# Optimization experiments

Hardware: AMD Instinct MI355X
Metric: run time of the kernel (lower is better)

The kernel has to match this reference:

```python
import jax, jax.numpy as jnp
import numpy as np

BETA = 0.25


def setup_inputs() -> dict:
    key = jax.random.key(0)
    k1, k2 = jax.random.split(key)
    ze = jax.random.normal(k1, (16, 64, 64, 64), dtype=jnp.float32)  # (B, L, H, W)
    # codebook init mirrors uniform_(-1/K, 1/K)
    K = 1024
    emb = jax.random.uniform(k2, (K, 64), dtype=jnp.float32, minval=-1.0 / K, maxval=1.0 / K)
    return {"ze": ze, "emb": emb}


def reference(ze, emb):
    B, L, H, W = ze.shape
    K = emb.shape[0]
    # (B, H, W, L) -> (N, L)
    zf = jnp.transpose(ze, (0, 2, 3, 1)).reshape(-1, L)
    # squared euclidean distances (N, K)
    d = (jnp.sum(zf * zf, axis=1, keepdims=True)
         + jnp.sum(emb * emb, axis=1)
         - 2.0 * zf @ emb.T)
    idx = jnp.argmin(d, axis=1)  # (N,)
    # direct gather == one-hot @ emb
    z_q = jnp.transpose(emb[idx].reshape(B, H, W, L), (0, 3, 1, 2))
    loss = (jnp.mean((jax.lax.stop_gradient(z_q) - ze) ** 2)
            + BETA * jnp.mean((z_q - jax.lax.stop_gradient(ze)) ** 2))
    # straight-through estimator
    z_q_st = ze + jax.lax.stop_gradient(z_q - ze)
    # perplexity of code usage
    counts = jnp.zeros((K,), dtype=zf.dtype).at[idx].add(1.0)
    e_mean = counts / zf.shape[0]
    perplexity = jnp.exp(-jnp.sum(e_mean * jnp.log(e_mean + 1e-10)))
    return z_q_st, loss, idx.reshape(-1, 1)
```

## Files before the change

kernel.cpp:

```cpp
#include <hip/hip_runtime.h>

typedef short bf16x8 __attribute__((ext_vector_type(8)));
typedef float f32x4  __attribute__((ext_vector_type(4)));

#define CAP 12

#define WS_LOSS 0
#define WS_DONE 8
#define WS_EN   64
#define WS_EBF  4160

#define L_EBF    0
#define L_MARG   131072
#define L_CCNT   132096
#define L_KCH    133120
#define L_CSLOT  134144
#define L_TOTAL  146432

__device__ __forceinline__ unsigned short f2bf(float f) {
    unsigned u = __float_as_uint(f);
    return (unsigned short)((u + 0x7fffu + ((u >> 16) & 1u)) >> 16);
}

__device__ __forceinline__ float np_pairwise_sumsq64(const float* a) {
    float r[8];
    #pragma unroll
    for (int j = 0; j < 8; ++j) r[j] = __fmul_rn(a[j], a[j]);
    #pragma unroll
    for (int i = 8; i < 64; i += 8)
        #pragma unroll
        for (int j = 0; j < 8; ++j)
            r[j] = __fadd_rn(r[j], __fmul_rn(a[i + j], a[i + j]));
    return __fadd_rn(
        __fadd_rn(__fadd_rn(r[0], r[1]), __fadd_rn(r[2], r[3])),
        __fadd_rn(__fadd_rn(r[4], r[5]), __fadd_rn(r[6], r[7])));
}

__global__ __launch_bounds__(256) void prep_kernel(
    const float* __restrict__ emb, unsigned short* __restrict__ ebf,
    float* __restrict__ en_t,
    float* __restrict__ loss, int* __restrict__ done)
{
    int k = blockIdx.x * 256 + threadIdx.x;
    if (k == 0) { *loss = 0.0f; *done = 0; }
    if (k < 1024) {
        float e[64];
        #pragma unroll
        for (int l = 0; l < 64; ++l) e[l] = emb[k * 64 + l];
        en_t[k] = np_pairwise_sumsq64(e);
        int tile = k >> 4, r = k & 15;
        #pragma unroll
        for (int j = 0; j < 8; ++j) {
            bf16x8 v;
            #pragma unroll
            for (int m = 0; m < 8; ++m) v[m] = (short)f2bf(e[j * 8 + m]);
            *(bf16x8*)(ebf + tile * 1024 + j * 128 + r * 8) = v;
        }
    }
}

__global__ __launch_bounds__(512, 2)
void vq_kernel(
    const float* __restrict__ ze, const float* __restrict__ emb,
    const unsigned short* __restrict__ ebf, const float* __restrict__ en_t,
    float* __restrict__ out_zq, float* __restrict__ out_idxf,
    float* __restrict__ loss, int* __restrict__ done,
    float* __restrict__ out_loss)
{
    extern __shared__ char smem[];
    unsigned short* ebf_l = (unsigned short*)(smem + L_EBF);
    float*          marg_l= (float*)(smem + L_MARG);
    int*            ccnt  = (int*)(smem + L_CCNT);
    int*            kch   = (int*)(smem + L_KCH);
    int*            cslot = (int*)(smem + L_CSLOT);

    const int t = threadIdx.x;
    const int n0 = blockIdx.x * 256;
    const int gbase = (n0 >> 12) * 262144 + (n0 & 4095);

    {
        const bf16x8* src = (const bf16x8*)ebf;
        bf16x8* dst = (bf16x8*)ebf_l;
        #pragma unroll 16
        for (int i = 0; i < 16; ++i) dst[t + i * 512] = src[t + i * 512];
    }

    const int wv = t >> 6, lane = t & 63;
    const int r = lane & 15, q = lane >> 4;
    const int wp = wv * 32;
    bf16x8 a[2][2];
    float sm[2] = {0.f, 0.f};
    #pragma unroll
    for (int rg = 0; rg < 2; ++rg) {
        const float* zb = ze + gbase + wp + rg * 16 + r;
        #pragma unroll
        for (int j = 0; j < 8; ++j) {
            const float v0 = zb[(q * 8 + j) * 4096];
            const float v1 = zb[(32 + q * 8 + j) * 4096];
            a[rg][0][j] = (short)f2bf(v0);
            a[rg][1][j] = (short)f2bf(v1);
            sm[rg] += fabsf(v0) + fabsf(v1);
        }
    }
    #pragma unroll
    for (int rg = 0; rg < 2; ++rg) {
        float s = sm[rg];
        s += __shfl_xor(s, 16, 64);
        s += __shfl_xor(s, 32, 64);
        if (q == 0) marg_l[wp + rg * 16 + r] = 1.67e-5f * s + 2.0e-4f;
    }
    if (t < 256) ccnt[t] = 0;
    __syncthreads();

    const unsigned short* bptr = ebf_l + q * 128 + r * 8;

    float rm[8];
    #pragma unroll
    for (int i = 0; i < 8; ++i) rm[i] = -1e30f;
    {
        bf16x8 pb0[8], pb1[8];
        #pragma unroll
        for (int i = 0; i < 8; ++i) {
            pb0[i] = *(const bf16x8*)(bptr + i * 1024);
            pb1[i] = *(const bf16x8*)(bptr + i * 1024 + 512);
        }
        #pragma unroll 8
        for (int tile = 0; tile < 64; ++tile) {
            bf16x8 b0 = pb0[tile & 7], b1 = pb1[tile & 7];
            int nt = tile + 8; if (nt > 63) nt = 63;
            pb0[tile & 7] = *(const bf16x8*)(bptr + nt * 1024);
            pb1[tile & 7] = *(const bf16x8*)(bptr + nt * 1024 + 512);
            #pragma unroll
            for (int rg = 0; rg < 2; ++rg) {
                f32x4 c = {0.f, 0.f, 0.f, 0.f};
                c = __builtin_amdgcn_mfma_f32_16x16x32_bf16(a[rg][0], b0, c, 0, 0, 0);
                c = __builtin_amdgcn_mfma_f32_16x16x32_bf16(a[rg][1], b1, c, 0, 0, 0);
                #pragma unroll
                for (int i = 0; i < 4; ++i)
                    rm[rg * 4 + i] = fmaxf(rm[rg * 4 + i], c[i]);
            }
        }
    }
    #pragma unroll
    for (int j = 0; j < 8; ++j) {
        float v = rm[j];
        v = fmaxf(v, __shfl_xor(v, 1, 16));
        v = fmaxf(v, __shfl_xor(v, 2, 16));
        v = fmaxf(v, __shfl_xor(v, 4, 16));
        v = fmaxf(v, __shfl_xor(v, 8, 16));
        rm[j] = v;
    }
    float thr[8];
    #pragma unroll
    for (int j = 0; j < 8; ++j) {
        const int row = wp + (j >> 2) * 16 + q * 4 + (j & 3);
        thr[j] = rm[j] - 0.5f * marg_l[row];
    }

    float z[64];
    {
        const int p = t >> 1;
        const float* zp = ze + gbase + p;
        #pragma unroll
        for (int l = 0; l < 64; ++l) z[l] = zp[l * 4096];
    }

    {
        bf16x8 pb0[8], pb1[8];
        #pragma unroll
        for (int i = 0; i < 8; ++i) {
            pb0[i] = *(const bf16x8*)(bptr + i * 1024);
            pb1[i] = *(const bf16x8*)(bptr + i * 1024 + 512);
        }
        #pragma unroll 8
        for (int tile = 0; tile < 64; ++tile) {
            bf16x8 b0 = pb0[tile & 7], b1 = pb1[tile & 7];
            int nt = tile + 8; if (nt > 63) nt = 63;
            pb0[tile & 7] = *(const bf16x8*)(bptr + nt * 1024);
            pb1[tile & 7] = *(const bf16x8*)(bptr + nt * 1024 + 512);
            const int code = tile * 16 + r;
            #pragma unroll
            for (int rg = 0; rg < 2; ++rg) {
                f32x4 c = {0.f, 0.f, 0.f, 0.f};
                c = __builtin_amdgcn_mfma_f32_16x16x32_bf16(a[rg][0], b0, c, 0, 0, 0);
                c = __builtin_amdgcn_mfma_f32_16x16x32_bf16(a[rg][1], b1, c, 0, 0, 0);
                #pragma unroll
                for (int i = 0; i < 4; ++i) {
                    if (c[i] >= thr[rg * 4 + i]) {
                        const int pp = wp + rg * 16 + q * 4 + i;
                        const int ci = atomicAdd(&ccnt[pp], 1);
                        if (ci < CAP) cslot[pp * CAP + ci] = code;
                    }
                }
            }
        }
    }
    __syncthreads();

    {
        const int p = t >> 1, cl = t & 1;
        int cnt = ccnt[p]; if (cnt > CAP) cnt = CAP;
        const float znorm = np_pairwise_sumsq64(z);
        float best = 1e30f; int bk = 1 << 20;
        int kcur = (cl < cnt) ? cslot[p * CAP + cl] : 0;
        for (int c = cl; c < cnt; c += 2) {
            const int k = kcur;
            const int ni = c + 2;
            kcur = (ni < cnt) ? cslot[p * CAP + ni] : 0;
            const float4* er = (const float4*)(emb + k * 64);
            float acc = 0.0f;
            #pragma unroll
            for (int jj = 0; jj < 16; ++jj) {
                const float4 v = er[jj];
                acc = fmaf(z[4 * jj + 0], v.x, acc);
                acc = fmaf(z[4 * jj + 1], v.y, acc);
                acc = fmaf(z[4 * jj + 2], v.z, acc);
                acc = fmaf(z[4 * jj + 3], v.w, acc);
            }
            const float sc = __fsub_rn(__fadd_rn(znorm, en_t[k]), __fmul_rn(2.0f, acc));
            if (sc < best || (sc == best && k < bk)) { best = sc; bk = k; }
        }
        const float ob = __shfl_xor(best, 1, 64);
        const int   ok = __shfl_xor(bk, 1, 64);
        if (ob < best || (ob == best && ok < bk)) { best = ob; bk = ok; }
        if (cl == 0) {
            kch[p] = bk;
            out_idxf[n0 + p] = (float)bk;
        }
    }
    __syncthreads();

    {
        const int p = t & 255, h = t >> 8;
        const int bk = kch[p];
        const float* er = emb + bk * 64 + h * 32;
        const float* zp = ze + gbase + p + (h * 32) * 4096;
        float* op = out_zq + gbase + p + (h * 32) * 4096;
        float ev[32], zv[32];
        #pragma unroll
        for (int j = 0; j < 32; ++j) ev[j] = er[j];
        #pragma unroll
        for (int j = 0; j < 32; ++j) zv[j] = zp[j * 4096];
        float ls = 0.0f;
        #pragma unroll
        for (int j = 0; j < 32; ++j) {
            op[j * 4096] = ev[j];
            const float d = ev[j] - zv[j];
            ls = fmaf(d, d, ls);
        }
        #pragma unroll
        for (int off = 32; off > 0; off >>= 1) ls += __shfl_down(ls, off, 64);
        if (lane == 0) atomicAdd(loss, ls);
    }

    __syncthreads();
    if (t == 0) {
        __threadfence();
        int old = atomicAdd(done, 1);
        if (old == (int)gridDim.x - 1) {
            __threadfence();
            float total = atomicAdd(loss, 0.0f);
            *out_loss = 1.25f * total / 4194304.0f;
        }
    }
}

extern "C" void kernel_launch(void* const* d_in, const int* in_sizes, int n_in,
                              void* d_out, int out_size, void* d_ws, size_t ws_size,
                              hipStream_t stream)
{
    const float* ze  = (const float*)d_in[0];
    const float* emb = (const float*)d_in[1];
    float* out = (float*)d_out;
    float* out_zq   = out;
    float* out_loss = out + 4194304;
    float* out_idxf = out + 4194305;

    char* w = (char*)d_ws;
    float*          ws_loss = (float*)(w + WS_LOSS);
    int*            ws_done = (int*)(w + WS_DONE);
    float*          ws_en   = (float*)(w + WS_EN);
    unsigned short* ebf     = (unsigned short*)(w + WS_EBF);

    static bool attr_set = false;
    if (!attr_set) {
        hipFuncSetAttribute((const void*)vq_kernel,
                            hipFuncAttributeMaxDynamicSharedMemorySize, L_TOTAL);
        attr_set = true;
    }

    prep_kernel<<<4, 256, 0, stream>>>(emb, ebf, ws_en, ws_loss, ws_done);
    vq_kernel<<<256, 512, L_TOTAL, stream>>>(ze, emb, ebf, ws_en, out_zq,
                                             out_idxf, ws_loss, ws_done, out_loss);
}
```

Before: 138.2 us.

## Split fused VQ kernel into distance, rescore, and epilogue kernels

The single fused kernel becomes three launches: a bf16 MFMA candidate-filter kernel that writes per-point candidate lists to global scratch (aliased into the z_q output buffer), an fp32 rescore kernel with one thread per point, and an epilogue that gathers codes, writes z_q and reduces the loss. This removes the 64-float z register array from the MFMA kernel and lets each phase use its own launch shape and occupancy. The cost is extra launches, a global round trip for candidate slots and indices, and a second read of ze.

```diff
diff --git a/kernel.cpp b/kernel.cpp
--- a/kernel.cpp
+++ b/kernel.cpp
@@ -10,12 +10,14 @@
 #define WS_EN   64
 #define WS_EBF  4160
 
-#define L_EBF    0
-#define L_MARG   131072
-#define L_CCNT   132096
-#define L_KCH    133120
-#define L_CSLOT  134144
-#define L_TOTAL  146432
+#define SLOT_OFF 0
+#define CNT_OFF  786432
+
+#define LD_EBF    0
+#define LD_MARG   131072
+#define LD_CCNT   132096
+#define LD_CSLOT  133120
+#define LD_TOTAL  145408
 
 __device__ __forceinline__ unsigned short f2bf(float f) {
     unsigned u = __float_as_uint(f);
@@ -60,19 +62,15 @@
 }
 
 __global__ __launch_bounds__(512, 2)
-void vq_kernel(
-    const float* __restrict__ ze, const float* __restrict__ emb,
-    const unsigned short* __restrict__ ebf, const float* __restrict__ en_t,
-    float* __restrict__ out_zq, float* __restrict__ out_idxf,
-    float* __restrict__ loss, int* __restrict__ done,
-    float* __restrict__ out_loss)
+void dist_kernel(
+    const float* __restrict__ ze, const unsigned short* __restrict__ ebf,
+    int* __restrict__ slot_g, int* __restrict__ cnt_g)
 {
     extern __shared__ char smem[];
-    unsigned short* ebf_l = (unsigned short*)(smem + L_EBF);
-    float*          marg_l= (float*)(smem + L_MARG);
-    int*            ccnt  = (int*)(smem + L_CCNT);
-    int*            kch   = (int*)(smem + L_KCH);
-    int*            cslot = (int*)(smem + L_CSLOT);
+    unsigned short* ebf_l = (unsigned short*)(smem + LD_EBF);
+    float*          marg_l= (float*)(smem + LD_MARG);
+    int*            ccnt  = (int*)(smem + LD_CCNT);
+    int*            cslot = (int*)(smem + LD_CSLOT);
 
     const int t = threadIdx.x;
     const int n0 = blockIdx.x * 256;
@@ -155,14 +153,6 @@
     for (int j = 0; j < 8; ++j) {
         const int row = wp + (j >> 2) * 16 + q * 4 + (j & 3);
         thr[j] = rm[j] - 0.5f * marg_l[row];
-    }
-
-    float z[64];
-    {
-        const int p = t >> 1;
-        const float* zp = ze + gbase + p;
-        #pragma unroll
-        for (int l = 0; l < 64; ++l) z[l] = zp[l * 4096];
     }
 
     {
@@ -197,61 +187,78 @@
     }
     __syncthreads();
 
-    {
-        const int p = t >> 1, cl = t & 1;
-        int cnt = ccnt[p]; if (cnt > CAP) cnt = CAP;
-        const float znorm = np_pairwise_sumsq64(z);
-        float best = 1e30f; int bk = 1 << 20;
-        int kcur = (cl < cnt) ? cslot[p * CAP + cl] : 0;
-        for (int c = cl; c < cnt; c += 2) {
-            const int k = kcur;
-            const int ni = c + 2;
-            kcur = (ni < cnt) ? cslot[p * CAP + ni] : 0;
-            const float4* er = (const float4*)(emb + k * 64);
-            float acc = 0.0f;
-            #pragma unroll
-            for (int jj = 0; jj < 16; ++jj) {
-                const float4 v = er[jj];
-                acc = fmaf(z[4 * jj + 0], v.x, acc);
-                acc = fmaf(z[4 * jj + 1], v.y, acc);
-                acc = fmaf(z[4 * jj + 2], v.z, acc);
-                acc = fmaf(z[4 * jj + 3], v.w, acc);
-            }
-            const float sc = __fsub_rn(__fadd_rn(znorm, en_t[k]), __fmul_rn(2.0f, acc));
-            if (sc < best || (sc == best && k < bk)) { best = sc; bk = k; }
-        }
-        const float ob = __shfl_xor(best, 1, 64);
-        const int   ok = __shfl_xor(bk, 1, 64);
-        if (ob < best || (ob == best && ok < bk)) { best = ob; bk = ok; }
-        if (cl == 0) {
-            kch[p] = bk;
-            out_idxf[n0 + p] = (float)bk;
-        }
-    }
-    __syncthreads();
-
-    {
-        const int p = t & 255, h = t >> 8;
-        const int bk = kch[p];
-        const float* er = emb + bk * 64 + h * 32;
-        const float* zp = ze + gbase + p + (h * 32) * 4096;
-        float* op = out_zq + gbase + p + (h * 32) * 4096;
-        float ev[32], zv[32];
-        #pragma unroll
-        for (int j = 0; j < 32; ++j) ev[j] = er[j];
-        #pragma unroll
-        for (int j = 0; j < 32; ++j) zv[j] = zp[j * 4096];
-        float ls = 0.0f;
-        #pragma unroll
-        for (int j = 0; j < 32; ++j) {
-            op[j * 4096] = ev[j];
-            const float d = ev[j] - zv[j];
-            ls = fmaf(d, d, ls);
-        }
-        #pragma unroll
-        for (int off = 32; off > 0; off >>= 1) ls += __shfl_down(ls, off, 64);
-        if (lane == 0) atomicAdd(loss, ls);
-    }
+    if (t < 256) {
+        const int P = n0 + t;
+        cnt_g[P] = ccnt[t];
+        const int4* s = (const int4*)(cslot + t * CAP);
+        int4* d = (int4*)(slot_g + P * CAP);
+        d[0] = s[0]; d[1] = s[1]; d[2] = s[2];
+    }
+}
+
+__global__ __launch_bounds__(256, 4)
+void rescore_kernel(
+    const float* __restrict__ ze, const float* __restrict__ emb,
+    const float* __restrict__ en_t,
+    const int* __restrict__ slot_g, const int* __restrict__ cnt_g,
+    float* __restrict__ out_idxf)
+{
+    const int P = blockIdx.x * 256 + threadIdx.x;
+    int cnt = cnt_g[P]; if (cnt > CAP) cnt = CAP;
+    const float* zp = ze + (P >> 12) * 262144 + (P & 4095);
+    float z[64];
+    #pragma unroll
+    for (int l = 0; l < 64; ++l) z[l] = zp[l * 4096];
+    const float znorm = np_pairwise_sumsq64(z);
+    float best = 1e30f; int bk = 1 << 20;
+    for (int c = 0; c < cnt; ++c) {
+        const int k = slot_g[P * CAP + c];
+        const float4* er = (const float4*)(emb + k * 64);
+        float acc = 0.0f;
+        #pragma unroll
+        for (int jj = 0; jj < 16; ++jj) {
+            const float4 v = er[jj];
+            acc = fmaf(z[4 * jj + 0], v.x, acc);
+            acc = fmaf(z[4 * jj + 1], v.y, acc);
+            acc = fmaf(z[4 * jj + 2], v.z, acc);
+            acc = fmaf(z[4 * jj + 3], v.w, acc);
+        }
+        const float sc = __fsub_rn(__fadd_rn(znorm, en_t[k]), __fmul_rn(2.0f, acc));
+        if (sc < best || (sc == best && k < bk)) { best = sc; bk = k; }
+    }
+    out_idxf[P] = (float)bk;
+}
+
+__global__ __launch_bounds__(512, 2)
+void epi_kernel(
+    const float* __restrict__ ze, const float* __restrict__ emb,
+    const float* __restrict__ out_idxf,
+    float* __restrict__ out_zq, float* __restrict__ loss,
+    int* __restrict__ done, float* __restrict__ out_loss)
+{
+    const int t = threadIdx.x, lane = t & 63;
+    const int n0 = blockIdx.x * 256;
+    const int gbase = (n0 >> 12) * 262144 + (n0 & 4095);
+    const int p = t & 255, h = t >> 8;
+    const int bk = (int)out_idxf[n0 + p];
+    const float* er = emb + bk * 64 + h * 32;
+    const float* zp = ze + gbase + p + (h * 32) * 4096;
+    float* op = out_zq + gbase + p + (h * 32) * 4096;
+    float ev[32], zv[32];
+    #pragma unroll
+    for (int j = 0; j < 32; ++j) ev[j] = er[j];
+    #pragma unroll
+    for (int j = 0; j < 32; ++j) zv[j] = zp[j * 4096];
+    float ls = 0.0f;
+    #pragma unroll
+    for (int j = 0; j < 32; ++j) {
+        op[j * 4096] = ev[j];
+        const float d = ev[j] - zv[j];
+        ls = fmaf(d, d, ls);
+    }
+    #pragma unroll
+    for (int off = 32; off > 0; off >>= 1) ls += __shfl_down(ls, off, 64);
+    if (lane == 0) atomicAdd(loss, ls);
 
     __syncthreads();
     if (t == 0) {
@@ -282,14 +289,20 @@
     float*          ws_en   = (float*)(w + WS_EN);
     unsigned short* ebf     = (unsigned short*)(w + WS_EBF);
 
+    int* slot_g = (int*)out_zq + SLOT_OFF;
+    int* cnt_g  = (int*)out_zq + CNT_OFF;
+
     static bool attr_set = false;
     if (!attr_set) {
-        hipFuncSetAttribute((const void*)vq_kernel,
-                            hipFuncAttributeMaxDynamicSharedMemorySize, L_TOTAL);
+        hipFuncSetAttribute((const void*)dist_kernel,
+                            hipFuncAttributeMaxDynamicSharedMemorySize, LD_TOTAL);
         attr_set = true;
     }
 
     prep_kernel<<<4, 256, 0, stream>>>(emb, ebf, ws_en, ws_loss, ws_done);
-    vq_kernel<<<256, 512, L_TOTAL, stream>>>(ze, emb, ebf, ws_en, out_zq,
-                                             out_idxf, ws_loss, ws_done, out_loss);
-}
+    dist_kernel<<<256, 512, LD_TOTAL, stream>>>(ze, ebf, slot_g, cnt_g);
+    rescore_kernel<<<256, 256, 0, stream>>>(ze, emb, ws_en, slot_g, cnt_g,
+                                            out_idxf);
+    epi_kernel<<<256, 512, 0, stream>>>(ze, emb, out_idxf, out_zq,
+                                        ws_loss, ws_done, out_loss);
+}
```

Result: slower. 149.8 us (+8.4%).
